# Performance work log

Hardware: AMD Instinct MI355X
Metric: run time of the kernel (lower is better)

Reference implementation:

```python
import jax, jax.numpy as jnp
import numpy as np

UNITS = 512
IN_DIM = 256


def setup_inputs() -> dict:
    key = jax.random.key(0)
    k1, k2, k3 = jax.random.split(key, 3)
    x = jax.random.normal(k1, (128, 512, IN_DIM), dtype=jnp.float32)
    # glorot_uniform for kernel
    lim = float(np.sqrt(6.0 / (IN_DIM + UNITS)))
    kernel = jax.random.uniform(k2, (IN_DIM, UNITS), minval=-lim, maxval=lim, dtype=jnp.float32)
    # orthogonal init for recurrent kernel
    a = jax.random.normal(k3, (UNITS, UNITS), dtype=jnp.float32)
    q, r = jnp.linalg.qr(a)
    recurrent_kernel = q * jnp.sign(jnp.diag(r))[None, :]
    bias = jnp.zeros((UNITS,), dtype=jnp.float32)
    return {"x": x, "kernel": kernel, "recurrent_kernel": recurrent_kernel, "bias": bias}


def reference(x, kernel, recurrent_kernel, bias):
    # h_t = tanh(x_t @ W_x + b + h_{t-1} @ W_h), return full sequence [B, T, U]
    B = x.shape[0]
    # Precompute input projection for all timesteps in one batched GEMM
    xp = jnp.einsum('btf,fu->btu', x, kernel) + bias  # [B, T, U]

    def step(h, xp_t):
        h_new = jnp.tanh(xp_t + h @ recurrent_kernel)
        return h_new, h_new

    h0 = jnp.zeros((B, UNITS), dtype=x.dtype)
    _, ys = jax.lax.scan(step, h0, jnp.swapaxes(xp, 0, 1))  # ys: [T, B, U]
    return jnp.swapaxes(ys, 0, 1)
```

## Files before the change

kernel.cpp:

```cpp
#include <hip/hip_runtime.h>
#include <math.h>


#define SENT 0xFFFFFFFFu
#define ALF(p)    __hip_atomic_load((p), __ATOMIC_RELAXED, __HIP_MEMORY_SCOPE_AGENT)
#define ASF(p, v) __hip_atomic_store((p), (v), __ATOMIC_RELAXED, __HIP_MEMORY_SCOPE_AGENT)
#define FMA4(A, W, H) { (A).x += (H)*(W).x; (A).y += (H)*(W).y; (A).z += (H)*(W).z; (A).w += (H)*(W).w; }

__global__ __launch_bounds__(256) void xp_gemm_sent(
    const float* __restrict__ x,
    const float* __restrict__ wx,
    const float* __restrict__ bias,
    float* __restrict__ xp,
    float* __restrict__ out)
{
    __shared__ float As[32][68];
    __shared__ float Bs[32][68];

    const int tid = threadIdx.x;
    const int m0 = blockIdx.y * 64;
    const int n0 = blockIdx.x * 64;
    const int tm = tid / 16;
    const int tn = tid % 16;

    {
        const float s = __uint_as_float(SENT);
        const float4 sv = make_float4(s, s, s, s);
        const int r = tid >> 4;
        const int c = (tid & 15) * 4;
        float* op = out + (size_t)m0 * 512 + n0;
        #pragma unroll
        for (int i = 0; i < 4; ++i)
            *(float4*)&op[(size_t)(r + 16 * i) * 512 + c] = sv;
    }

    float acc[4][4] = {};

    for (int k0 = 0; k0 < 256; k0 += 32) {
        {
            const int kk = tid % 32, r0 = tid / 32;
            #pragma unroll
            for (int rr = 0; rr < 8; ++rr)
                As[kk][r0 + rr * 8] = x[(size_t)(m0 + r0 + rr * 8) * 256 + (k0 + kk)];
        }
        {
            const int nn = tid % 64, r0 = tid / 64;
            #pragma unroll
            for (int rr = 0; rr < 8; ++rr)
                Bs[r0 + rr * 4][nn] = wx[(size_t)(k0 + r0 + rr * 4) * 512 + (n0 + nn)];
        }
        __syncthreads();

        #pragma unroll
        for (int kk = 0; kk < 32; ++kk) {
            const float4 a = *(const float4*)&As[kk][tm * 4];
            const float4 b = *(const float4*)&Bs[kk][tn * 4];
            const float av[4] = {a.x, a.y, a.z, a.w};
            const float bv[4] = {b.x, b.y, b.z, b.w};
            #pragma unroll
            for (int i = 0; i < 4; ++i)
                #pragma unroll
                for (int j = 0; j < 4; ++j)
                    acc[i][j] += av[i] * bv[j];
        }
        __syncthreads();
    }

    #pragma unroll
    for (int i = 0; i < 4; ++i)
        #pragma unroll
        for (int j = 0; j < 4; ++j)
            xp[(size_t)(m0 + tm * 4 + i) * 512 + (n0 + tn * 4 + j)] =
                acc[i][j] + bias[n0 + tn * 4 + j];
}

__global__ __launch_bounds__(1024) void rnn_scan9(
    const float* __restrict__ wh,
    const float* __restrict__ xp,
    float* __restrict__ out)
{
    __shared__ float h_lds[2][512];
    __shared__ float red[32][2][128];

    const int tid = threadIdx.x;
    const int us  = blockIdx.x >> 6;
    const int bg  = blockIdx.x & 63;
    const int u0  = us * 128;
    const int g   = tid & 31;
    const int s   = tid >> 5;
    const int kbase = s * 16;
    const size_t seq = 512 * 512;

    const float* wr = &wh[(size_t)kbase * 512 + (u0 + 4 * g)];
    const float4 w0  = *(const float4*)(wr + 0  * 512);
    const float4 w1  = *(const float4*)(wr + 1  * 512);
    const float4 w2  = *(const float4*)(wr + 2  * 512);
    const float4 w3  = *(const float4*)(wr + 3  * 512);
    const float4 w4  = *(const float4*)(wr + 4  * 512);
    const float4 w5  = *(const float4*)(wr + 5  * 512);
    const float4 w6  = *(const float4*)(wr + 6  * 512);
    const float4 w7  = *(const float4*)(wr + 7  * 512);
    const float4 w8  = *(const float4*)(wr + 8  * 512);
    const float4 w9  = *(const float4*)(wr + 9  * 512);
    const float4 w10 = *(const float4*)(wr + 10 * 512);
    const float4 w11 = *(const float4*)(wr + 11 * 512);
    const float4 w12 = *(const float4*)(wr + 12 * 512);
    const float4 w13 = *(const float4*)(wr + 13 * 512);
    const float4 w14 = *(const float4*)(wr + 14 * 512);
    const float4 w15 = *(const float4*)(wr + 15 * 512);

    const int ru = tid & 127;
    const int rb = (tid >> 7) & 1;
    const float* xpp = xp + (size_t)(bg * 2 + rb) * seq + u0 + ru;
    float*       hop = out + (size_t)(bg * 2 + rb) * seq + u0 + ru;

    const int sb   = (tid >= 384) ? 1 : 0;
    const int srem = tid - sb * 384;
    const int shk  = (srem < u0) ? srem : srem + 128;
    const float* pollp = out + (size_t)(bg * 2 + sb) * seq + shk;

    for (int t = 0; t < 512; ++t) {
        float xpv = 0.0f;
        if (tid < 256) xpv = xpp[(size_t)t * 512];

        if (t == 0) {
            ((float*)h_lds)[tid] = 0.0f;
        } else if (tid < 768) {
            const float* p = pollp + (size_t)(t - 1) * 512;
            float v = ALF(p);
            int it = 0;
            while (__float_as_uint(v) == SENT && ++it < (1 << 22)) {
                if (it > 32) __builtin_amdgcn_s_sleep(1);
                v = ALF(p);
            }
            h_lds[sb][shk] = v;
        }
        __syncthreads();

        float4 a0 = make_float4(0.f, 0.f, 0.f, 0.f);
        float4 a1 = make_float4(0.f, 0.f, 0.f, 0.f);
        const float* hb0 = &h_lds[0][kbase];
        const float* hb1 = &h_lds[1][kbase];
        #define STEP4(W0, W1, W2, W3, OFF) { \
            const float4 h0 = *(const float4*)(hb0 + (OFF)); \
            const float4 h1 = *(const float4*)(hb1 + (OFF)); \
            FMA4(a0, W0, h0.x) FMA4(a0, W1, h0.y) FMA4(a0, W2, h0.z) FMA4(a0, W3, h0.w) \
            FMA4(a1, W0, h1.x) FMA4(a1, W1, h1.y) FMA4(a1, W2, h1.z) FMA4(a1, W3, h1.w) }
        STEP4(w0,  w1,  w2,  w3,  0)
        STEP4(w4,  w5,  w6,  w7,  4)
        STEP4(w8,  w9,  w10, w11, 8)
        STEP4(w12, w13, w14, w15, 12)
        #undef STEP4

        *(float4*)&red[s][0][4 * g] = a0;
        *(float4*)&red[s][1][4 * g] = a1;
        __syncthreads();

        if (tid < 256) {
            float r = xpv;
            #pragma unroll
            for (int ss = 0; ss < 32; ++ss) r += red[ss][rb][ru];
            const float hn = tanhf(r);
            ASF(hop + (size_t)t * 512, hn);
            h_lds[rb][u0 + ru] = hn;
        }
    }
}

__global__ __launch_bounds__(256) void xp_gemm_plain(
    const float* __restrict__ x, const float* __restrict__ wx,
    const float* __restrict__ bias, float* __restrict__ xp)
{
    __shared__ float As[32][68];
    __shared__ float Bs[32][68];
    const int tid = threadIdx.x;
    const int m0 = blockIdx.y * 64;
    const int n0 = blockIdx.x * 64;
    const int tm = tid / 16;
    const int tn = tid % 16;
    float acc[4][4] = {};
    for (int k0 = 0; k0 < 256; k0 += 32) {
        {
            const int kk = tid % 32, r0 = tid / 32;
            #pragma unroll
            for (int rr = 0; rr < 8; ++rr)
                As[kk][r0 + rr * 8] = x[(size_t)(m0 + r0 + rr * 8) * 256 + (k0 + kk)];
        }
        {
            const int nn = tid % 64, r0 = tid / 64;
            #pragma unroll
            for (int rr = 0; rr < 8; ++rr)
                Bs[r0 + rr * 4][nn] = wx[(size_t)(k0 + r0 + rr * 4) * 512 + (n0 + nn)];
        }
        __syncthreads();
        #pragma unroll
        for (int kk = 0; kk < 32; ++kk) {
            const float4 a = *(const float4*)&As[kk][tm * 4];
            const float4 b = *(const float4*)&Bs[kk][tn * 4];
            const float av[4] = {a.x, a.y, a.z, a.w};
            const float bv[4] = {b.x, b.y, b.z, b.w};
            #pragma unroll
            for (int i = 0; i < 4; ++i)
                #pragma unroll
                for (int j = 0; j < 4; ++j)
                    acc[i][j] += av[i] * bv[j];
        }
        __syncthreads();
    }
    #pragma unroll
    for (int i = 0; i < 4; ++i)
        #pragma unroll
        for (int j = 0; j < 4; ++j)
            xp[(size_t)(m0 + tm * 4 + i) * 512 + (n0 + tn * 4 + j)] =
                acc[i][j] + bias[n0 + tn * 4 + j];
}

__global__ __launch_bounds__(1024, 4) void rnn_scan2(
    const float* __restrict__ wh, float* __restrict__ out)
{
    __shared__ float h_lds[2][512];
    __shared__ float red[8][2][512];
    const int tid = threadIdx.x;
    const int g = tid & 127;
    const int s = tid >> 7;
    const int b = tid >> 9;
    const int u = tid & 511;
    float* seqb = out + (size_t)(2 * blockIdx.x + b) * 512 * 512;
    h_lds[b][u] = 0.0f;
    __syncthreads();
    const float4* __restrict__ whv = (const float4*)wh;
    const int kbase = s * 64;
    for (int t = 0; t < 512; ++t) {
        const float xpv = seqb[(size_t)t * 512 + u];
        float4 a0 = make_float4(0.f, 0.f, 0.f, 0.f);
        float4 a1 = make_float4(0.f, 0.f, 0.f, 0.f);
        #pragma unroll 4
        for (int kk = 0; kk < 64; kk += 4) {
            const int k = kbase + kk;
            const float4 h0 = *(const float4*)&h_lds[0][k];
            const float4 h1 = *(const float4*)&h_lds[1][k];
            const float4 v0 = whv[(k + 0) * 128 + g];
            const float4 v1 = whv[(k + 1) * 128 + g];
            const float4 v2 = whv[(k + 2) * 128 + g];
            const float4 v3 = whv[(k + 3) * 128 + g];
            FMA4(a0, v0, h0.x) FMA4(a0, v1, h0.y) FMA4(a0, v2, h0.z) FMA4(a0, v3, h0.w)
            FMA4(a1, v0, h1.x) FMA4(a1, v1, h1.y) FMA4(a1, v2, h1.z) FMA4(a1, v3, h1.w)
        }
        *(float4*)&red[s][0][4 * g] = a0;
        *(float4*)&red[s][1][4 * g] = a1;
        __syncthreads();
        float r = xpv;
        #pragma unroll
        for (int ss = 0; ss < 8; ++ss) r += red[ss][b][u];
        const float hn = tanhf(r);
        h_lds[b][u] = hn;
        seqb[(size_t)t * 512 + u] = hn;
        __syncthreads();
    }
}

extern "C" void kernel_launch(void* const* d_in, const int* in_sizes, int n_in,
                              void* d_out, int out_size, void* d_ws, size_t ws_size,
                              hipStream_t stream) {
    const float* x    = (const float*)d_in[0];
    const float* wx   = (const float*)d_in[1];
    const float* wh   = (const float*)d_in[2];
    const float* bias = (const float*)d_in[3];
    float* out = (float*)d_out;

    const size_t xp_bytes = (size_t)128 * 512 * 512 * sizeof(float);
    dim3 g1(512 / 64, 65536 / 64);

    if (d_ws != nullptr && ws_size >= xp_bytes) {
        xp_gemm_sent<<<g1, 256, 0, stream>>>(x, wx, bias, (float*)d_ws, out);
        rnn_scan9<<<256, 1024, 0, stream>>>(wh, (const float*)d_ws, out);
    } else {
        xp_gemm_plain<<<g1, 256, 0, stream>>>(x, wx, bias, out);
        rnn_scan2<<<64, 1024, 0, stream>>>(wh, out);
    }
}
```

Baseline: 1.290 ms.

## Use bf16 MFMA for input projection and regroup scan blocks by batch

Replaces the fp32 SIMT input-projection GEMM with a bf16 MFMA kernel using 128x64 tiles, converting x and W_x to bf16 in shared memory. The aim is to cut GEMM time, at the cost of reduced precision in xp. The scan kernel remaps block indices so the four unit-slices of a batch group get adjacent block IDs, which should make them co-resident. It also changes the spin-wait to sleep on every poll and adds a trailing barrier per timestep.

```diff
diff --git a/kernel.cpp b/kernel.cpp
--- a/kernel.cpp
+++ b/kernel.cpp
@@ -7,74 +7,111 @@
 #define ASF(p, v) __hip_atomic_store((p), (v), __ATOMIC_RELAXED, __HIP_MEMORY_SCOPE_AGENT)
 #define FMA4(A, W, H) { (A).x += (H)*(W).x; (A).y += (H)*(W).y; (A).z += (H)*(W).z; (A).w += (H)*(W).w; }
 
-__global__ __launch_bounds__(256) void xp_gemm_sent(
+typedef __attribute__((ext_vector_type(8))) short bfrag8;
+typedef __attribute__((ext_vector_type(4))) float ffrag4;
+
+__device__ __forceinline__ unsigned pack2bf(float a, float b) {
+    unsigned ua = __float_as_uint(a), ub = __float_as_uint(b);
+    ua += 0x7FFFu + ((ua >> 16) & 1u);
+    ub += 0x7FFFu + ((ub >> 16) & 1u);
+    return (ua >> 16) | (ub & 0xFFFF0000u);
+}
+__device__ __forceinline__ short f2bf(float f) {
+    unsigned u = __float_as_uint(f);
+    u += 0x7FFFu + ((u >> 16) & 1u);
+    return (short)(u >> 16);
+}
+
+__global__ __launch_bounds__(256) void xp_gemm_mfma(
     const float* __restrict__ x,
     const float* __restrict__ wx,
     const float* __restrict__ bias,
     float* __restrict__ xp,
     float* __restrict__ out)
 {
-    __shared__ float As[32][68];
-    __shared__ float Bs[32][68];
-
-    const int tid = threadIdx.x;
-    const int m0 = blockIdx.y * 64;
-    const int n0 = blockIdx.x * 64;
-    const int tm = tid / 16;
-    const int tn = tid % 16;
+    __shared__ short Abf[128][40];
+    __shared__ short Bbf[64][40];
+
+    const int tid  = threadIdx.x;
+    const int lane = tid & 63;
+    const int w    = tid >> 6;
+    const int n0   = blockIdx.x * 64;
+    const int m0   = blockIdx.y * 128;
 
     {
-        const float s = __uint_as_float(SENT);
-        const float4 sv = make_float4(s, s, s, s);
-        const int r = tid >> 4;
-        const int c = (tid & 15) * 4;
-        float* op = out + (size_t)m0 * 512 + n0;
-        #pragma unroll
-        for (int i = 0; i < 4; ++i)
-            *(float4*)&op[(size_t)(r + 16 * i) * 512 + c] = sv;
-    }
-
-    float acc[4][4] = {};
-
-    for (int k0 = 0; k0 < 256; k0 += 32) {
+        const float s1 = __uint_as_float(SENT);
+        const float4 sv = make_float4(s1, s1, s1, s1);
+        const int r = tid >> 1, hf = (tid & 1) * 32;
+        float* op = out + (size_t)(m0 + r) * 512 + n0 + hf;
+        #pragma unroll
+        for (int i = 0; i < 8; ++i) *(float4*)(op + 4 * i) = sv;
+    }
+
+    float bsv[4];
+    #pragma unroll
+    for (int ct = 0; ct < 4; ++ct) bsv[ct] = bias[n0 + ct * 16 + (lane & 15)];
+
+    ffrag4 acc[2][4];
+    #pragma unroll
+    for (int i = 0; i < 2; ++i)
+        #pragma unroll
+        for (int j = 0; j < 4; ++j)
+            acc[i][j] = (ffrag4){0.f, 0.f, 0.f, 0.f};
+
+    const int arow  = tid >> 1;
+    const int ahalf = (tid & 1) * 16;
+    const int bk    = tid >> 3;
+    const int bn    = (tid & 7) * 8;
+
+    for (int kt = 0; kt < 8; ++kt) {
         {
-            const int kk = tid % 32, r0 = tid / 32;
-            #pragma unroll
-            for (int rr = 0; rr < 8; ++rr)
-                As[kk][r0 + rr * 8] = x[(size_t)(m0 + r0 + rr * 8) * 256 + (k0 + kk)];
+            const float* src = x + (size_t)(m0 + arow) * 256 + kt * 32 + ahalf;
+            const float4 f0 = *(const float4*)(src + 0);
+            const float4 f1 = *(const float4*)(src + 4);
+            const float4 f2 = *(const float4*)(src + 8);
+            const float4 f3 = *(const float4*)(src + 12);
+            unsigned* dst = (unsigned*)&Abf[arow][ahalf];
+            dst[0] = pack2bf(f0.x, f0.y); dst[1] = pack2bf(f0.z, f0.w);
+            dst[2] = pack2bf(f1.x, f1.y); dst[3] = pack2bf(f1.z, f1.w);
+            dst[4] = pack2bf(f2.x, f2.y); dst[5] = pack2bf(f2.z, f2.w);
+            dst[6] = pack2bf(f3.x, f3.y); dst[7] = pack2bf(f3.z, f3.w);
         }
         {
-            const int nn = tid % 64, r0 = tid / 64;
-            #pragma unroll
-            for (int rr = 0; rr < 8; ++rr)
-                Bs[r0 + rr * 4][nn] = wx[(size_t)(k0 + r0 + rr * 4) * 512 + (n0 + nn)];
-        }
-        __syncthreads();
-
-        #pragma unroll
-        for (int kk = 0; kk < 32; ++kk) {
-            const float4 a = *(const float4*)&As[kk][tm * 4];
-            const float4 b = *(const float4*)&Bs[kk][tn * 4];
-            const float av[4] = {a.x, a.y, a.z, a.w};
-            const float bv[4] = {b.x, b.y, b.z, b.w};
-            #pragma unroll
-            for (int i = 0; i < 4; ++i)
-                #pragma unroll
-                for (int j = 0; j < 4; ++j)
-                    acc[i][j] += av[i] * bv[j];
-        }
-        __syncthreads();
-    }
-
+            const float* src = wx + (size_t)(kt * 32 + bk) * 512 + n0 + bn;
+            const float4 f0 = *(const float4*)(src + 0);
+            const float4 f1 = *(const float4*)(src + 4);
+            Bbf[bn + 0][bk] = f2bf(f0.x); Bbf[bn + 1][bk] = f2bf(f0.y);
+            Bbf[bn + 2][bk] = f2bf(f0.z); Bbf[bn + 3][bk] = f2bf(f0.w);
+            Bbf[bn + 4][bk] = f2bf(f1.x); Bbf[bn + 5][bk] = f2bf(f1.y);
+            Bbf[bn + 6][bk] = f2bf(f1.z); Bbf[bn + 7][bk] = f2bf(f1.w);
+        }
+        __syncthreads();
+
+        const int kq = (lane >> 4) * 8;
+        const bfrag8 a0 = *(const bfrag8*)&Abf[w * 32 + (lane & 15)][kq];
+        const bfrag8 a1 = *(const bfrag8*)&Abf[w * 32 + 16 + (lane & 15)][kq];
+        #pragma unroll
+        for (int ct = 0; ct < 4; ++ct) {
+            const bfrag8 bf = *(const bfrag8*)&Bbf[ct * 16 + (lane & 15)][kq];
+            acc[0][ct] = __builtin_amdgcn_mfma_f32_16x16x32_bf16(a0, bf, acc[0][ct], 0, 0, 0);
+            acc[1][ct] = __builtin_amdgcn_mfma_f32_16x16x32_bf16(a1, bf, acc[1][ct], 0, 0, 0);
+        }
+        __syncthreads();
+    }
+
+    const int col = lane & 15;
+    const int rg  = (lane >> 4) * 4;
     #pragma unroll
-    for (int i = 0; i < 4; ++i)
-        #pragma unroll
-        for (int j = 0; j < 4; ++j)
-            xp[(size_t)(m0 + tm * 4 + i) * 512 + (n0 + tn * 4 + j)] =
-                acc[i][j] + bias[n0 + tn * 4 + j];
-}
-
-__global__ __launch_bounds__(1024) void rnn_scan9(
+    for (int rt = 0; rt < 2; ++rt)
+        #pragma unroll
+        for (int ct = 0; ct < 4; ++ct)
+            #pragma unroll
+            for (int r = 0; r < 4; ++r)
+                xp[(size_t)(m0 + w * 32 + rt * 16 + rg + r) * 512 + n0 + ct * 16 + col]
+                    = acc[rt][ct][r] + bsv[ct];
+}
+
+__global__ __launch_bounds__(1024) void rnn_scan4(
     const float* __restrict__ wh,
     const float* __restrict__ xp,
     float* __restrict__ out)
@@ -83,8 +120,8 @@
     __shared__ float red[32][2][128];
 
     const int tid = threadIdx.x;
-    const int us  = blockIdx.x >> 6;
-    const int bg  = blockIdx.x & 63;
+    const int us  = blockIdx.x & 3;
+    const int bg  = blockIdx.x >> 2;
     const int u0  = us * 128;
     const int g   = tid & 31;
     const int s   = tid >> 5;
@@ -127,12 +164,13 @@
             ((float*)h_lds)[tid] = 0.0f;
         } else if (tid < 768) {
             const float* p = pollp + (size_t)(t - 1) * 512;
-            float v = ALF(p);
-            int it = 0;
-            while (__float_as_uint(v) == SENT && ++it < (1 << 22)) {
-                if (it > 32) __builtin_amdgcn_s_sleep(1);
+            float v;
+            int cnt = 0;
+            do {
                 v = ALF(p);
-            }
+                if (__float_as_uint(v) != SENT) break;
+                __builtin_amdgcn_s_sleep(1);
+            } while (++cnt < (1 << 20));
             h_lds[sb][shk] = v;
         }
         __syncthreads();
@@ -161,9 +199,10 @@
             #pragma unroll
             for (int ss = 0; ss < 32; ++ss) r += red[ss][rb][ru];
             const float hn = tanhf(r);
+            h_lds[rb][u0 + ru] = hn;
             ASF(hop + (size_t)t * 512, hn);
-            h_lds[rb][u0 + ru] = hn;
-        }
+        }
+        __syncthreads();
     }
 }
 
@@ -269,12 +308,13 @@
     float* out = (float*)d_out;
 
     const size_t xp_bytes = (size_t)128 * 512 * 512 * sizeof(float);
-    dim3 g1(512 / 64, 65536 / 64);
 
     if (d_ws != nullptr && ws_size >= xp_bytes) {
-        xp_gemm_sent<<<g1, 256, 0, stream>>>(x, wx, bias, (float*)d_ws, out);
-        rnn_scan9<<<256, 1024, 0, stream>>>(wh, (const float*)d_ws, out);
+        dim3 gm(512 / 64, 65536 / 128);
+        xp_gemm_mfma<<<gm, 256, 0, stream>>>(x, wx, bias, (float*)d_ws, out);
+        rnn_scan4<<<256, 1024, 0, stream>>>(wh, (const float*)d_ws, out);
     } else {
+        dim3 g1(512 / 64, 65536 / 64);
         xp_gemm_plain<<<g1, 256, 0, stream>>>(x, wx, bias, out);
         rnn_scan2<<<64, 1024, 0, stream>>>(wh, out);
     }
```

New measurement: 1.081 ms, median of 2. 16.2% less time.
